# Kernel optimization log

Hardware: AMD Instinct MI355X
Metric: run time of the kernel (lower is better)

The kernel has to match this reference:

```python
import jax, jax.numpy as jnp
import numpy as np

B, T, D, F, E = 4, 2048, 1024, 2048, 16  # batch, seq, hidden, intermediate, experts


def setup_inputs() -> dict:
    key = jax.random.key(0)
    k0, k1, k2, k3 = jax.random.split(key, 4)
    x = jax.random.normal(k0, (B, T, D), dtype=jnp.float32)
    # gate: torch Linear(D, E, bias=False); store as [D, E] so logits = h @ Wg
    Wg = jax.random.normal(k1, (D, E), dtype=jnp.float32) * 0.02
    # experts: kaiming_uniform(a=sqrt(5)) -> U(-1/sqrt(fan_in), 1/sqrt(fan_in))
    W1 = jax.random.uniform(k2, (E, D, F), minval=-1.0, maxval=1.0, dtype=jnp.float32) / np.sqrt(D)
    W2 = jax.random.uniform(k3, (E, F, D), minval=-1.0, maxval=1.0, dtype=jnp.float32) / np.sqrt(F)
    return {"x": x, "Wg": Wg, "W1": W1, "W2": W2}


def reference(x, Wg, W1, W2):
    b, t, d = x.shape
    e = Wg.shape[1]
    h = x.reshape(-1, d)                     # [N, D], N = b*t tokens
    n = h.shape[0]

    # --- gate: top-2 routing with fp32 softmax over the 2 selected logits ---
    logits = h @ Wg                          # [N, E]
    scores, idx = jax.lax.top_k(logits, 2)   # [N, 2]
    scores = jax.nn.softmax(scores.astype(jnp.float32), axis=-1).astype(x.dtype)

    # dense combine weights [N, E]: weight of expert e for each token (0 if not routed)
    combine = jnp.zeros((n, e), dtype=x.dtype).at[
        jnp.arange(n)[:, None], idx
    ].add(scores)

    # --- dispatch/combine: scan over experts, weight-accumulate outputs ---
    # Mathematically identical to the masked-loop original: tokens not routed
    # to expert e contribute with weight 0.
    def step(acc, params):
        W1e, W2e, w = params                  # [D,F], [F,D], [N]
        out = jax.nn.silu(h @ W1e) @ W2e      # [N, D]
        return acc + w[:, None] * out, None

    y, _ = jax.lax.scan(step, jnp.zeros_like(h), (W1, W2, combine.T))
    return y.reshape(b, t, d)
```

## Files before the change

### kernel.cpp

```cpp
#include <hip/hip_runtime.h>
#include <hip/hip_bf16.h>

#define NTOK 8192
#define DDIM 1024
#define FDIM 2048
#define NEXP 16
#define CAP   1280
#define CAPRG 80

#define WS_COUNTS 0
#define WS_TOKL   4096
#define WS_WGTL   (4096 + NTOK*NEXP*4)
#define WS_POS    (4096 + 2*NTOK*NEXP*4)
#define WS_TW     (4096 + 2*NTOK*NEXP*4 + NTOK*8)
#define WS2_XG   (size_t)(2u<<20)
#define WS2_W1   (size_t)(42u<<20)
#define WS2_W2   (size_t)(106u<<20)
#define WS2_UG   (size_t)(170u<<20)

typedef short bf16x8 __attribute__((ext_vector_type(8)));
typedef float f32x4  __attribute__((ext_vector_type(4)));

__device__ __forceinline__ unsigned short f2bf(float f) {
  unsigned int u = __builtin_bit_cast(unsigned int, f);
  u += 0x7fffu + ((u >> 16) & 1u);
  return (unsigned short)(u >> 16);
}
__device__ __forceinline__ unsigned int pk2(float a, float b) {
  return (unsigned int)f2bf(a) | ((unsigned int)f2bf(b) << 16);
}
__device__ __forceinline__ float bf2f(unsigned int u) {
  return __builtin_bit_cast(float, u << 16);
}
__device__ __forceinline__ float silu_f(float s) {
  return s / (1.f + __expf(-s));
}
__device__ __forceinline__ void gld_lds16(const void* g, void* l) {
  __builtin_amdgcn_global_load_lds((const __attribute__((address_space(1))) void*)g,
                                   (__attribute__((address_space(3))) void*)l, 16, 0, 0);
}

__global__ __launch_bounds__(1024) void gate_kernel(
    const float* __restrict__ x, const float* __restrict__ Wg,
    int* __restrict__ counts, int* __restrict__ tokl, float* __restrict__ wgtl,
    int* __restrict__ pos, float* __restrict__ tw) {
  __shared__ float WgT[NEXP][DDIM];
  __shared__ int   se[32];
  __shared__ float swt[32];
  __shared__ int   sbase[16];
  int tid = threadIdx.x;
#pragma unroll
  for (int i = 0; i < 4; ++i) {
    int i4 = i * 1024 + tid;
    float4 v = ((const float4*)Wg)[i4];
    int k = i4 >> 2;
    int e0 = (i4 * 4) & 15;
    WgT[e0][k] = v.x; WgT[e0 + 1][k] = v.y;
    WgT[e0 + 2][k] = v.z; WgT[e0 + 3][k] = v.w;
  }
  __syncthreads();

  int wid = tid >> 6, lane = tid & 63;
  int tok = blockIdx.x * 16 + wid;
  const float* xr = x + (size_t)tok * DDIM;
  float xv[16];
#pragma unroll
  for (int j = 0; j < 16; ++j) xv[j] = xr[lane + 64 * j];
  float lg[NEXP];
#pragma unroll
  for (int e = 0; e < NEXP; ++e) {
    float s = 0.f;
#pragma unroll
    for (int j = 0; j < 16; ++j) s += xv[j] * WgT[e][lane + 64 * j];
#pragma unroll
    for (int off = 32; off > 0; off >>= 1) s += __shfl_xor(s, off);
    lg[e] = s;
  }
  int e0 = 0; float b0 = lg[0];
#pragma unroll
  for (int e = 1; e < NEXP; ++e) if (lg[e] > b0) { b0 = lg[e]; e0 = e; }
  int e1 = -1; float b1 = -3.4e38f;
#pragma unroll
  for (int e = 0; e < NEXP; ++e) if (e != e0 && lg[e] > b1) { b1 = lg[e]; e1 = e; }
  float t = expf(b1 - b0);
  float w0 = 1.f / (1.f + t);
  float w1 = t / (1.f + t);
  if (lane == 0) {
    se[wid * 2] = e0;  swt[wid * 2] = w0;
    se[wid * 2 + 1] = e1;  swt[wid * 2 + 1] = w1;
  }
  __syncthreads();

  if (tid < 16) {
    int cnt = 0;
#pragma unroll
    for (int i = 0; i < 32; ++i) cnt += (se[i] == tid) ? 1 : 0;
    sbase[tid] = cnt ? atomicAdd(&counts[tid * 16], cnt) : 0;
    int slot = sbase[tid];
    for (int i = 0; i < 32; ++i) {
      if (se[i] == tid) {
        int tk = blockIdx.x * 16 + (i >> 1);
        float w = swt[i];
        if (slot < CAP) { tokl[tid * NTOK + slot] = tk; wgtl[tid * NTOK + slot] = w; }
        pos[tk * 2 + (i & 1)] = (slot < CAP) ? (tid * CAP + slot) : -1;
        tw[tk * 2 + (i & 1)] = w;
        slot++;
      }
    }
  }
}

__global__ __launch_bounds__(256) void convert_w2(
    const float* __restrict__ W1, const float* __restrict__ W2,
    unsigned short* __restrict__ W1s, unsigned short* __restrict__ W2s) {
  __shared__ float tile[32][133];
  int b = blockIdx.x;
  bool isw2 = b >= 8192;
  int bb = isw2 ? b - 8192 : b;
  int e = bb >> 9;
  int r = bb & 511;
  int t = threadIdx.x;
  const float* src;
  int kk, cb, C;
  if (!isw2) {
    kk = r >> 4; cb = r & 15; C = FDIM;
    src = W1 + ((size_t)e << 21) + (size_t)(kk * 32) * FDIM + cb * 128;
  } else {
    kk = r >> 3; cb = r & 7; C = DDIM;
    src = W2 + ((size_t)e << 21) + (size_t)(kk * 32) * DDIM + cb * 128;
  }
  int c4 = (t & 31) * 4, rr0 = t >> 5;
#pragma unroll
  for (int rd = 0; rd < 4; ++rd) {
    int rr = rr0 + rd * 8;
    float4 v = *(const float4*)(src + (size_t)rr * C + c4);
    tile[rr][c4] = v.x; tile[rr][c4 + 1] = v.y;
    tile[rr][c4 + 2] = v.z; tile[rr][c4 + 3] = v.w;
  }
  __syncthreads();
  int w = t >> 6, lane = t & 63, llo = lane & 15, lhi = lane >> 4;
#pragma unroll
  for (int u = 0; u < 2; ++u) {
    int c2 = w * 2 + u;
    float v[8];
#pragma unroll
    for (int j = 0; j < 8; ++j) {
      int row = isw2 ? (4 * lhi + (j & 3) + 16 * (j >> 2)) : (lhi * 8 + j);
      v[j] = tile[row][c2 * 16 + llo];
    }
    uint4 o;
    o.x = pk2(v[0], v[1]); o.y = pk2(v[2], v[3]);
    o.z = pk2(v[4], v[5]); o.w = pk2(v[6], v[7]);
    size_t gid = isw2 ? (((size_t)e * 64 + kk) * 64 + (cb * 8 + c2))
                      : (((size_t)e * 128 + (cb * 8 + c2)) * 32 + kk);
    *(uint4*)((isw2 ? W2s : W1s) + (gid << 9) + lane * 8) = o;
  }
}

__global__ __launch_bounds__(512) void gather_x(
    const float* __restrict__ x, const int* __restrict__ counts,
    const int* __restrict__ tokl, unsigned short* __restrict__ Xg) {
  int chunk = blockIdx.x * 8 + (threadIdx.x >> 6);
  int lane = threadIdx.x & 63, llo = lane & 15, lhi = lane >> 4;
  int kb = chunk & 31;
  int rg = (chunk >> 5) % CAPRG;
  int e = chunk / (CAPRG * 32);
  int cnt = min(counts[e * 16], CAP);
  int slot = rg * 16 + llo;
  uint4 o = {0u, 0u, 0u, 0u};
  if (slot < cnt) {
    int tok = tokl[e * NTOK + slot];
    const float* p = x + (size_t)tok * DDIM + kb * 32 + lhi * 8;
    float4 a = *(const float4*)p, b2 = *(const float4*)(p + 4);
    o.x = pk2(a.x, a.y); o.y = pk2(a.z, a.w);
    o.z = pk2(b2.x, b2.y); o.w = pk2(b2.z, b2.w);
  }
  *(uint4*)(Xg + ((size_t)chunk << 9) + lane * 8) = o;
}

__global__ __launch_bounds__(512, 2) void g1(
    const unsigned short* __restrict__ W1s, const unsigned short* __restrict__ Xg,
    const int* __restrict__ counts, unsigned short* __restrict__ Ug) {
  int id = blockIdx.x;
  int e = ((id & 7) << 1) | ((id >> 3) & 1);
  int rest = id >> 4;
  int ft = rest & 7;
  int tt = rest >> 3;
  int cnt = min(counts[e * 16], CAP);
  if (tt * 256 >= cnt) return;

  extern __shared__ char smem[];
  int tid = threadIdx.x, wid = tid >> 6, lane = tid & 63;
  int llo = lane & 15, lhi = lane >> 4;
  int wm = wid >> 2, wn = wid & 3;

  f32x4 acc[8][4];
#pragma unroll
  for (int i = 0; i < 8; ++i)
#pragma unroll
    for (int j = 0; j < 4; ++j) acc[i][j] = (f32x4){0.f, 0.f, 0.f, 0.f};

  const size_t abase = ((size_t)e * 128 + ft * 16) * 32;
  const size_t bbase = ((size_t)e * CAPRG + tt * 16) * 32;

#define G1_STAGE(B, T)                                                          \
  {                                                                             \
    char* dst = smem + (B) * 65536;                                             \
    _Pragma("unroll")                                                           \
    for (int i = 0; i < 8; ++i) {                                               \
      int c = wid * 8 + i;                                                      \
      if (c < 32) {                                                             \
        int fl = c >> 1, kkl = c & 1;                                           \
        gld_lds16(W1s + ((abase + (size_t)fl * 32 + (T) * 2 + kkl) << 9) + lane * 8, \
                  dst + c * 1024);                                              \
      } else {                                                                  \
        int cb = c - 32, rgl = cb >> 1, kkl = cb & 1;                           \
        gld_lds16(Xg + ((bbase + (size_t)rgl * 32 + (T) * 2 + kkl) << 9) + lane * 8, \
                  dst + c * 1024);                                              \
      }                                                                         \
    }                                                                           \
  }

  G1_STAGE(0, 0);
  asm volatile("s_waitcnt vmcnt(0)" ::: "memory");
  __builtin_amdgcn_s_barrier();
  int cur = 0;
  for (int t = 0; t < 16; ++t) {
    if (t < 15) G1_STAGE(cur ^ 1, t + 1);
    const char* bufc = smem + cur * 65536;
#pragma unroll
    for (int kk = 0; kk < 2; ++kk) {
      bf16x8 af[8], bx[4];
#pragma unroll
      for (int fi = 0; fi < 8; ++fi)
        af[fi] = *(const bf16x8*)(bufc + (((wm * 8 + fi) * 2 + kk) << 10) + lane * 16);
#pragma unroll
      for (int ti = 0; ti < 4; ++ti)
        bx[ti] = *(const bf16x8*)(bufc + 32768 + (((wn * 4 + ti) * 2 + kk) << 10) + lane * 16);
#pragma unroll
      for (int fi = 0; fi < 8; ++fi)
#pragma unroll
        for (int ti = 0; ti < 4; ++ti)
          acc[fi][ti] = __builtin_amdgcn_mfma_f32_16x16x32_bf16(af[fi], bx[ti], acc[fi][ti], 0, 0, 0);
    }
    asm volatile("s_waitcnt vmcnt(0)" ::: "memory");
    __builtin_amdgcn_s_barrier();
    cur ^= 1;
  }

#pragma unroll
  for (int ti = 0; ti < 4; ++ti) {
    int rg = tt * 16 + wn * 4 + ti;
#pragma unroll
    for (int p = 0; p < 4; ++p) {
      int fo = ft * 8 + wm * 4 + p;
      uint4 v;
      v.x = pk2(silu_f(acc[2 * p][ti][0]), silu_f(acc[2 * p][ti][1]));
      v.y = pk2(silu_f(acc[2 * p][ti][2]), silu_f(acc[2 * p][ti][3]));
      v.z = pk2(silu_f(acc[2 * p + 1][ti][0]), silu_f(acc[2 * p + 1][ti][1]));
      v.w = pk2(silu_f(acc[2 * p + 1][ti][2]), silu_f(acc[2 * p + 1][ti][3]));
      *(uint4*)(Ug + ((((size_t)e * CAPRG + rg) * 64 + fo) << 9) + lane * 8) = v;
    }
  }
}

__global__ __launch_bounds__(512, 2) void g2(
    const unsigned short* __restrict__ W2s, const unsigned short* __restrict__ Ug,
    const int* __restrict__ counts, unsigned short* __restrict__ Yp) {
  int id = blockIdx.x;
  int e = ((id & 7) << 1) | ((id >> 3) & 1);
  int rest = id >> 4;
  int dt = rest & 3;
  int tt = rest >> 2;
  int cnt = min(counts[e * 16], CAP);
  int tb0 = tt * 256;
  if (tb0 >= cnt) return;

  extern __shared__ char smem[];
  int tid = threadIdx.x;
  int wid = tid >> 6, lane = tid & 63, llo = lane & 15, lhi = lane >> 4;
  int wm = wid >> 2, wn = wid & 3;

  f32x4 acc[8][4];
#pragma unroll
  for (int i = 0; i < 8; ++i)
#pragma unroll
    for (int j = 0; j < 4; ++j) acc[i][j] = (f32x4){0.f, 0.f, 0.f, 0.f};

  const size_t abase = (size_t)e * 4096 + dt * 16;
  const size_t bbase = ((size_t)e * CAPRG + tt * 16) * 64;

#define G2_STAGE(B, T)                                                          \
  {                                                                             \
    char* dst = smem + (B) * 65536;                                             \
    _Pragma("unroll")                                                           \
    for (int i = 0; i < 8; ++i) {                                               \
      int c = wid * 8 + i;                                                      \
      if (c < 32) {                                                             \
        int cl = c >> 1, kkl = c & 1;                                           \
        gld_lds16(W2s + ((abase + (size_t)((T) * 2 + kkl) * 64 + cl) << 9) + lane * 8, \
                  dst + c * 1024);                                              \
      } else {                                                                  \
        int cb = c - 32, rgl = cb >> 1, kkl = cb & 1;                           \
        gld_lds16(Ug + ((bbase + (size_t)rgl * 64 + (T) * 2 + kkl) << 9) + lane * 8, \
                  dst + c * 1024);                                              \
      }                                                                         \
    }                                                                           \
  }

  G2_STAGE(0, 0);
  asm volatile("s_waitcnt vmcnt(0)" ::: "memory");
  __builtin_amdgcn_s_barrier();
  int cur = 0;
  for (int t = 0; t < 32; ++t) {
    if (t < 31) G2_STAGE(cur ^ 1, t + 1);
    const char* bufc = smem + cur * 65536;
#pragma unroll
    for (int kk = 0; kk < 2; ++kk) {
      bf16x8 aw[8], bu[4];
#pragma unroll
      for (int di = 0; di < 8; ++di)
        aw[di] = *(const bf16x8*)(bufc + (((wm * 8 + di) * 2 + kk) << 10) + lane * 16);
#pragma unroll
      for (int ti = 0; ti < 4; ++ti)
        bu[ti] = *(const bf16x8*)(bufc + 32768 + (((wn * 4 + ti) * 2 + kk) << 10) + lane * 16);
#pragma unroll
      for (int di = 0; di < 8; ++di)
#pragma unroll
        for (int ti = 0; ti < 4; ++ti)
          acc[di][ti] = __builtin_amdgcn_mfma_f32_16x16x32_bf16(aw[di], bu[ti], acc[di][ti], 0, 0, 0);
    }
    asm volatile("s_waitcnt vmcnt(0)" ::: "memory");
    __builtin_amdgcn_s_barrier();
    cur ^= 1;
  }

#pragma unroll
  for (int di = 0; di < 8; ++di)
#pragma unroll
    for (int ti = 0; ti < 4; ++ti) {
      int slot = tb0 + wn * 64 + ti * 16 + llo;
      int d = dt * 256 + wm * 128 + di * 16 + 4 * lhi;
      uint2 v;
      v.x = pk2(acc[di][ti][0], acc[di][ti][1]);
      v.y = pk2(acc[di][ti][2], acc[di][ti][3]);
      *(uint2*)(Yp + (((size_t)e * CAP + slot) << 10) + d) = v;
    }
}

__global__ __launch_bounds__(256) void combine_k(
    const unsigned short* __restrict__ Yp, const int* __restrict__ pos,
    const float* __restrict__ tw, float* __restrict__ out) {
  int gid = blockIdx.x * 256 + threadIdx.x;
  int tok = gid >> 7, oct = gid & 127;
  int p0 = pos[tok * 2], p1 = pos[tok * 2 + 1];
  float w0 = tw[tok * 2], w1 = tw[tok * 2 + 1];
  float r[8];
#pragma unroll
  for (int j = 0; j < 8; ++j) r[j] = 0.f;
  if (p0 >= 0) {
    uint4 a = *(const uint4*)(Yp + (((size_t)p0) << 10) + (oct << 3));
    unsigned int w[4] = {a.x, a.y, a.z, a.w};
#pragma unroll
    for (int h = 0; h < 4; ++h) {
      r[2 * h]     += w0 * bf2f(w[h] & 0xffffu);
      r[2 * h + 1] += w0 * bf2f(w[h] >> 16);
    }
  }
  if (p1 >= 0) {
    uint4 a = *(const uint4*)(Yp + (((size_t)p1) << 10) + (oct << 3));
    unsigned int w[4] = {a.x, a.y, a.z, a.w};
#pragma unroll
    for (int h = 0; h < 4; ++h) {
      r[2 * h]     += w1 * bf2f(w[h] & 0xffffu);
      r[2 * h + 1] += w1 * bf2f(w[h] >> 16);
    }
  }
  float4 o0 = {r[0], r[1], r[2], r[3]}, o1 = {r[4], r[5], r[6], r[7]};
  float* dst = out + ((size_t)tok << 10) + (oct << 3);
  *(float4*)dst = o0;
  *(float4*)(dst + 4) = o1;
}

extern "C" void kernel_launch(void* const* d_in, const int* in_sizes, int n_in,
                              void* d_out, int out_size, void* d_ws, size_t ws_size,
                              hipStream_t stream) {
  const float* x  = (const float*)d_in[0];
  const float* Wg = (const float*)d_in[1];
  const float* W1 = (const float*)d_in[2];
  const float* W2 = (const float*)d_in[3];
  float* out = (float*)d_out;

  int*   counts = (int*)((char*)d_ws + WS_COUNTS);
  int*   tokl   = (int*)((char*)d_ws + WS_TOKL);
  float* wgtl   = (float*)((char*)d_ws + WS_WGTL);
  int*   pos    = (int*)((char*)d_ws + WS_POS);
  float* tw     = (float*)((char*)d_ws + WS_TW);
  unsigned short* XgN = (unsigned short*)((char*)d_ws + WS2_XG);
  unsigned short* W1n = (unsigned short*)((char*)d_ws + WS2_W1);
  unsigned short* W2n = (unsigned short*)((char*)d_ws + WS2_W2);
  unsigned short* UgN = (unsigned short*)((char*)d_ws + WS2_UG);

  hipMemsetAsync(counts, 0, 1024, stream);

  gate_kernel<<<NTOK / 16, 1024, 0, stream>>>(x, Wg, counts, tokl, wgtl, pos, tw);
  convert_w2<<<16384, 256, 0, stream>>>(W1, W2, W1n, W2n);
  gather_x<<<5120, 512, 0, stream>>>(x, counts, tokl, XgN);

  hipFuncSetAttribute((const void*)g1,
                      hipFuncAttributeMaxDynamicSharedMemorySize, 131072);
  hipFuncSetAttribute((const void*)g2,
                      hipFuncAttributeMaxDynamicSharedMemorySize, 131072);
  g1<<<NEXP * 8 * 5, 512, 131072, stream>>>(W1n, XgN, counts, UgN);
  g2<<<NEXP * 4 * 5, 512, 131072, stream>>>(W2n, UgN, counts, XgN );
  combine_k<<<4096, 256, 0, stream>>>(XgN , pos, tw, out);
}
```

Measured before the change: 376.2 us.

## Relax load waits with partial vmcnt and remap blocks to group experts per XCD

The prefetch-wait point moves to the top of each iteration, where it uses vmcnt(8) so the next stage's loads stay in flight while the current stage is consumed. The end-of-iteration wait becomes lgkmcnt(0), which protects the LDS reads before the buffer is overwritten. Block ids are also remapped so that each XCD handles two whole experts, with their tiles laid out contiguously, which should improve L2 reuse of expert weights. The risk is a subtle ordering hazard if the vmcnt accounting does not match the number of loads each thread issues per stage.

```diff
diff --git a/kernel.cpp b/kernel.cpp
--- a/kernel.cpp
+++ b/kernel.cpp
@@ -182,10 +182,11 @@
     const unsigned short* __restrict__ W1s, const unsigned short* __restrict__ Xg,
     const int* __restrict__ counts, unsigned short* __restrict__ Ug) {
   int id = blockIdx.x;
-  int e = ((id & 7) << 1) | ((id >> 3) & 1);
-  int rest = id >> 4;
-  int ft = rest & 7;
-  int tt = rest >> 3;
+  int xcd = id & 7, q = id >> 3;
+  int r = q / 40, s = q % 40;
+  int e = xcd * 2 + r;
+  int ft = s & 7;
+  int tt = s >> 3;
   int cnt = min(counts[e * 16], CAP);
   if (tt * 256 >= cnt) return;
 
@@ -222,11 +223,15 @@
   }
 
   G1_STAGE(0, 0);
-  asm volatile("s_waitcnt vmcnt(0)" ::: "memory");
-  __builtin_amdgcn_s_barrier();
   int cur = 0;
   for (int t = 0; t < 16; ++t) {
-    if (t < 15) G1_STAGE(cur ^ 1, t + 1);
+    if (t < 15) {
+      G1_STAGE(cur ^ 1, t + 1);
+      asm volatile("s_waitcnt vmcnt(8)" ::: "memory");
+    } else {
+      asm volatile("s_waitcnt vmcnt(0)" ::: "memory");
+    }
+    __builtin_amdgcn_s_barrier();
     const char* bufc = smem + cur * 65536;
 #pragma unroll
     for (int kk = 0; kk < 2; ++kk) {
@@ -243,7 +248,7 @@
         for (int ti = 0; ti < 4; ++ti)
           acc[fi][ti] = __builtin_amdgcn_mfma_f32_16x16x32_bf16(af[fi], bx[ti], acc[fi][ti], 0, 0, 0);
     }
-    asm volatile("s_waitcnt vmcnt(0)" ::: "memory");
+    asm volatile("s_waitcnt lgkmcnt(0)" ::: "memory");
     __builtin_amdgcn_s_barrier();
     cur ^= 1;
   }
@@ -268,10 +273,11 @@
     const unsigned short* __restrict__ W2s, const unsigned short* __restrict__ Ug,
     const int* __restrict__ counts, unsigned short* __restrict__ Yp) {
   int id = blockIdx.x;
-  int e = ((id & 7) << 1) | ((id >> 3) & 1);
-  int rest = id >> 4;
-  int dt = rest & 3;
-  int tt = rest >> 2;
+  int xcd = id & 7, q = id >> 3;
+  int r = q / 20, s = q % 20;
+  int e = xcd * 2 + r;
+  int dt = s & 3;
+  int tt = s >> 2;
   int cnt = min(counts[e * 16], CAP);
   int tb0 = tt * 256;
   if (tb0 >= cnt) return;
@@ -309,11 +315,15 @@
   }
 
   G2_STAGE(0, 0);
-  asm volatile("s_waitcnt vmcnt(0)" ::: "memory");
-  __builtin_amdgcn_s_barrier();
   int cur = 0;
   for (int t = 0; t < 32; ++t) {
-    if (t < 31) G2_STAGE(cur ^ 1, t + 1);
+    if (t < 31) {
+      G2_STAGE(cur ^ 1, t + 1);
+      asm volatile("s_waitcnt vmcnt(8)" ::: "memory");
+    } else {
+      asm volatile("s_waitcnt vmcnt(0)" ::: "memory");
+    }
+    __builtin_amdgcn_s_barrier();
     const char* bufc = smem + cur * 65536;
 #pragma unroll
     for (int kk = 0; kk < 2; ++kk) {
@@ -330,7 +340,7 @@
         for (int ti = 0; ti < 4; ++ti)
           acc[di][ti] = __builtin_amdgcn_mfma_f32_16x16x32_bf16(aw[di], bu[ti], acc[di][ti], 0, 0, 0);
     }
-    asm volatile("s_waitcnt vmcnt(0)" ::: "memory");
+    asm volatile("s_waitcnt lgkmcnt(0)" ::: "memory");
     __builtin_amdgcn_s_barrier();
     cur ^= 1;
   }
```

Result: no change. 373.9 us (-0.6%).

## Halve GEMM output tiles in g1/g2 to double block count and occupancy

Applied to the files above, without the earlier changes.

Both expert GEMM kernels now compute 128x256 output tiles instead of 256x256, with a single k-chunk per stage and 48KB of LDS double buffering in place of 128KB. This doubles the grid size and permits four blocks per CU, aiming to fill the 256 CUs better given the small per-expert token counts. The cost is lower arithmetic intensity per block, twice the barriers per K, and more redundant loading of the token operand.

```diff
diff --git a/kernel.cpp b/kernel.cpp
--- a/kernel.cpp
+++ b/kernel.cpp
@@ -178,71 +178,65 @@
   *(uint4*)(Xg + ((size_t)chunk << 9) + lane * 8) = o;
 }
 
-__global__ __launch_bounds__(512, 2) void g1(
+__global__ __launch_bounds__(512, 4) void g1(
     const unsigned short* __restrict__ W1s, const unsigned short* __restrict__ Xg,
     const int* __restrict__ counts, unsigned short* __restrict__ Ug) {
   int id = blockIdx.x;
   int e = ((id & 7) << 1) | ((id >> 3) & 1);
   int rest = id >> 4;
-  int ft = rest & 7;
-  int tt = rest >> 3;
+  int ft = rest & 15;
+  int tt = rest >> 4;
   int cnt = min(counts[e * 16], CAP);
   if (tt * 256 >= cnt) return;
 
   extern __shared__ char smem[];
   int tid = threadIdx.x, wid = tid >> 6, lane = tid & 63;
   int llo = lane & 15, lhi = lane >> 4;
-  int wm = wid >> 2, wn = wid & 3;
-
-  f32x4 acc[8][4];
-#pragma unroll
-  for (int i = 0; i < 8; ++i)
+  int fm = wid >> 2, wn = wid & 3;
+
+  f32x4 acc[4][4];
+#pragma unroll
+  for (int i = 0; i < 4; ++i)
 #pragma unroll
     for (int j = 0; j < 4; ++j) acc[i][j] = (f32x4){0.f, 0.f, 0.f, 0.f};
 
-  const size_t abase = ((size_t)e * 128 + ft * 16) * 32;
+  const size_t abase = ((size_t)e * 128 + ft * 8) * 32;
   const size_t bbase = ((size_t)e * CAPRG + tt * 16) * 32;
 
-#define G1_STAGE(B, T)                                                          \
+#define G1_STAGE(DST, T)                                                        \
   {                                                                             \
-    char* dst = smem + (B) * 65536;                                             \
     _Pragma("unroll")                                                           \
-    for (int i = 0; i < 8; ++i) {                                               \
-      int c = wid * 8 + i;                                                      \
-      if (c < 32) {                                                             \
-        int fl = c >> 1, kkl = c & 1;                                           \
-        gld_lds16(W1s + ((abase + (size_t)fl * 32 + (T) * 2 + kkl) << 9) + lane * 8, \
-                  dst + c * 1024);                                              \
+    for (int i = 0; i < 3; ++i) {                                               \
+      int c = wid * 3 + i;                                                      \
+      if (c < 8) {                                                              \
+        gld_lds16(W1s + ((abase + (size_t)c * 32 + (T)) << 9) + lane * 8,       \
+                  (DST) + c * 1024);                                            \
       } else {                                                                  \
-        int cb = c - 32, rgl = cb >> 1, kkl = cb & 1;                           \
-        gld_lds16(Xg + ((bbase + (size_t)rgl * 32 + (T) * 2 + kkl) << 9) + lane * 8, \
-                  dst + c * 1024);                                              \
+        gld_lds16(Xg + ((bbase + (size_t)(c - 8) * 32 + (T)) << 9) + lane * 8,  \
+                  (DST) + c * 1024);                                            \
       }                                                                         \
     }                                                                           \
   }
 
-  G1_STAGE(0, 0);
+  G1_STAGE(smem, 0);
   asm volatile("s_waitcnt vmcnt(0)" ::: "memory");
   __builtin_amdgcn_s_barrier();
   int cur = 0;
-  for (int t = 0; t < 16; ++t) {
-    if (t < 15) G1_STAGE(cur ^ 1, t + 1);
-    const char* bufc = smem + cur * 65536;
-#pragma unroll
-    for (int kk = 0; kk < 2; ++kk) {
-      bf16x8 af[8], bx[4];
-#pragma unroll
-      for (int fi = 0; fi < 8; ++fi)
-        af[fi] = *(const bf16x8*)(bufc + (((wm * 8 + fi) * 2 + kk) << 10) + lane * 16);
+  for (int t = 0; t < 32; ++t) {
+    if (t < 31) G1_STAGE(smem + (cur ^ 1) * 24576, t + 1);
+    const char* bufc = smem + cur * 24576;
+    bf16x8 af[4], bx[4];
+#pragma unroll
+    for (int fi = 0; fi < 4; ++fi)
+      af[fi] = *(const bf16x8*)(bufc + ((fm * 4 + fi) << 10) + lane * 16);
+#pragma unroll
+    for (int ti = 0; ti < 4; ++ti)
+      bx[ti] = *(const bf16x8*)(bufc + 8192 + ((wn * 4 + ti) << 10) + lane * 16);
+#pragma unroll
+    for (int fi = 0; fi < 4; ++fi)
 #pragma unroll
       for (int ti = 0; ti < 4; ++ti)
-        bx[ti] = *(const bf16x8*)(bufc + 32768 + (((wn * 4 + ti) * 2 + kk) << 10) + lane * 16);
-#pragma unroll
-      for (int fi = 0; fi < 8; ++fi)
-#pragma unroll
-        for (int ti = 0; ti < 4; ++ti)
-          acc[fi][ti] = __builtin_amdgcn_mfma_f32_16x16x32_bf16(af[fi], bx[ti], acc[fi][ti], 0, 0, 0);
-    }
+        acc[fi][ti] = __builtin_amdgcn_mfma_f32_16x16x32_bf16(af[fi], bx[ti], acc[fi][ti], 0, 0, 0);
     asm volatile("s_waitcnt vmcnt(0)" ::: "memory");
     __builtin_amdgcn_s_barrier();
     cur ^= 1;
@@ -252,8 +246,8 @@
   for (int ti = 0; ti < 4; ++ti) {
     int rg = tt * 16 + wn * 4 + ti;
 #pragma unroll
-    for (int p = 0; p < 4; ++p) {
-      int fo = ft * 8 + wm * 4 + p;
+    for (int p = 0; p < 2; ++p) {
+      int fo = ft * 4 + fm * 2 + p;
       uint4 v;
       v.x = pk2(silu_f(acc[2 * p][ti][0]), silu_f(acc[2 * p][ti][1]));
       v.y = pk2(silu_f(acc[2 * p][ti][2]), silu_f(acc[2 * p][ti][3]));
@@ -264,14 +258,14 @@
   }
 }
 
-__global__ __launch_bounds__(512, 2) void g2(
+__global__ __launch_bounds__(512, 4) void g2(
     const unsigned short* __restrict__ W2s, const unsigned short* __restrict__ Ug,
     const int* __restrict__ counts, unsigned short* __restrict__ Yp) {
   int id = blockIdx.x;
   int e = ((id & 7) << 1) | ((id >> 3) & 1);
   int rest = id >> 4;
-  int dt = rest & 3;
-  int tt = rest >> 2;
+  int dt = rest & 7;
+  int tt = rest >> 3;
   int cnt = min(counts[e * 16], CAP);
   int tb0 = tt * 256;
   if (tb0 >= cnt) return;
@@ -279,68 +273,61 @@
   extern __shared__ char smem[];
   int tid = threadIdx.x;
   int wid = tid >> 6, lane = tid & 63, llo = lane & 15, lhi = lane >> 4;
-  int wm = wid >> 2, wn = wid & 3;
-
-  f32x4 acc[8][4];
-#pragma unroll
-  for (int i = 0; i < 8; ++i)
+  int dm = wid >> 2, wn = wid & 3;
+
+  f32x4 acc[4][4];
+#pragma unroll
+  for (int i = 0; i < 4; ++i)
 #pragma unroll
     for (int j = 0; j < 4; ++j) acc[i][j] = (f32x4){0.f, 0.f, 0.f, 0.f};
 
-  const size_t abase = (size_t)e * 4096 + dt * 16;
   const size_t bbase = ((size_t)e * CAPRG + tt * 16) * 64;
 
-#define G2_STAGE(B, T)                                                          \
+#define G2_STAGE(DST, T)                                                        \
   {                                                                             \
-    char* dst = smem + (B) * 65536;                                             \
     _Pragma("unroll")                                                           \
-    for (int i = 0; i < 8; ++i) {                                               \
-      int c = wid * 8 + i;                                                      \
-      if (c < 32) {                                                             \
-        int cl = c >> 1, kkl = c & 1;                                           \
-        gld_lds16(W2s + ((abase + (size_t)((T) * 2 + kkl) * 64 + cl) << 9) + lane * 8, \
-                  dst + c * 1024);                                              \
+    for (int i = 0; i < 3; ++i) {                                               \
+      int c = wid * 3 + i;                                                      \
+      if (c < 8) {                                                              \
+        gld_lds16(W2s + ((((size_t)e * 64 + (T)) * 64 + dt * 8 + c) << 9) + lane * 8, \
+                  (DST) + c * 1024);                                            \
       } else {                                                                  \
-        int cb = c - 32, rgl = cb >> 1, kkl = cb & 1;                           \
-        gld_lds16(Ug + ((bbase + (size_t)rgl * 64 + (T) * 2 + kkl) << 9) + lane * 8, \
-                  dst + c * 1024);                                              \
+        gld_lds16(Ug + ((bbase + (size_t)(c - 8) * 64 + (T)) << 9) + lane * 8,  \
+                  (DST) + c * 1024);                                            \
       }                                                                         \
     }                                                                           \
   }
 
-  G2_STAGE(0, 0);
+  G2_STAGE(smem, 0);
   asm volatile("s_waitcnt vmcnt(0)" ::: "memory");
   __builtin_amdgcn_s_barrier();
   int cur = 0;
-  for (int t = 0; t < 32; ++t) {
-    if (t < 31) G2_STAGE(cur ^ 1, t + 1);
-    const char* bufc = smem + cur * 65536;
-#pragma unroll
-    for (int kk = 0; kk < 2; ++kk) {
-      bf16x8 aw[8], bu[4];
-#pragma unroll
-      for (int di = 0; di < 8; ++di)
-        aw[di] = *(const bf16x8*)(bufc + (((wm * 8 + di) * 2 + kk) << 10) + lane * 16);
+  for (int t = 0; t < 64; ++t) {
+    if (t < 63) G2_STAGE(smem + (cur ^ 1) * 24576, t + 1);
+    const char* bufc = smem + cur * 24576;
+    bf16x8 aw[4], bu[4];
+#pragma unroll
+    for (int di = 0; di < 4; ++di)
+      aw[di] = *(const bf16x8*)(bufc + ((dm * 4 + di) << 10) + lane * 16);
+#pragma unroll
+    for (int ti = 0; ti < 4; ++ti)
+      bu[ti] = *(const bf16x8*)(bufc + 8192 + ((wn * 4 + ti) << 10) + lane * 16);
+#pragma unroll
+    for (int di = 0; di < 4; ++di)
 #pragma unroll
       for (int ti = 0; ti < 4; ++ti)
-        bu[ti] = *(const bf16x8*)(bufc + 32768 + (((wn * 4 + ti) * 2 + kk) << 10) + lane * 16);
-#pragma unroll
-      for (int di = 0; di < 8; ++di)
-#pragma unroll
-        for (int ti = 0; ti < 4; ++ti)
-          acc[di][ti] = __builtin_amdgcn_mfma_f32_16x16x32_bf16(aw[di], bu[ti], acc[di][ti], 0, 0, 0);
-    }
+        acc[di][ti] = __builtin_amdgcn_mfma_f32_16x16x32_bf16(aw[di], bu[ti], acc[di][ti], 0, 0, 0);
     asm volatile("s_waitcnt vmcnt(0)" ::: "memory");
     __builtin_amdgcn_s_barrier();
     cur ^= 1;
   }
 
 #pragma unroll
-  for (int di = 0; di < 8; ++di)
+  for (int di = 0; di < 4; ++di)
 #pragma unroll
     for (int ti = 0; ti < 4; ++ti) {
       int slot = tb0 + wn * 64 + ti * 16 + llo;
-      int d = dt * 256 + wm * 128 + di * 16 + 4 * lhi;
+      int d = dt * 128 + dm * 64 + di * 16 + 4 * lhi;
       uint2 v;
       v.x = pk2(acc[di][ti][0], acc[di][ti][1]);
       v.y = pk2(acc[di][ti][2], acc[di][ti][3]);
@@ -408,10 +395,10 @@
   gather_x<<<5120, 512, 0, stream>>>(x, counts, tokl, XgN);
 
   hipFuncSetAttribute((const void*)g1,
-                      hipFuncAttributeMaxDynamicSharedMemorySize, 131072);
+                      hipFuncAttributeMaxDynamicSharedMemorySize, 49152);
   hipFuncSetAttribute((const void*)g2,
-                      hipFuncAttributeMaxDynamicSharedMemorySize, 131072);
-  g1<<<NEXP * 8 * 5, 512, 131072, stream>>>(W1n, XgN, counts, UgN);
-  g2<<<NEXP * 4 * 5, 512, 131072, stream>>>(W2n, UgN, counts, XgN );
+                      hipFuncAttributeMaxDynamicSharedMemorySize, 49152);
+  g1<<<NEXP * 16 * 5, 512, 49152, stream>>>(W1n, XgN, counts, UgN);
+  g2<<<NEXP * 8 * 5, 512, 49152, stream>>>(W2n, UgN, counts, XgN );
   combine_k<<<4096, 256, 0, stream>>>(XgN , pos, tw, out);
 }
```

Result: faster. 365.7 us (-2.8%).
